# Kernel tuning notes

Measured on AMD Instinct MI355X. Metric: run time of the kernel, lower is better.

## Reference

```python
import jax, jax.numpy as jnp
import numpy as np

K = 3
PAD = 1
EPS = 1e-5


def _conv2d(x, w, b):
    y = jax.lax.conv_general_dilated(x, w, window_strides=(1, 1), padding='SAME',
                                     dimension_numbers=('NCHW', 'OIHW', 'NCHW'))
    return y + b[None, :, None, None]


def _bn(x, g, beta, m, v):
    inv = jax.lax.rsqrt(v + EPS)
    return (x - m[None, :, None, None]) * (g * inv)[None, :, None, None] + beta[None, :, None, None]


def _deform_conv2d(x, offset, w, b):
    # torchvision deform_conv2d (v1, no mask), stride=1, pad=1, 3x3 kernel.
    B, Cin, H, W = x.shape
    Cout = w.shape[0]
    # offset: [B, 2*K*K, H, W] -> (dy, dx) per kernel tap
    off = offset.reshape(B, K * K, 2, H, W)
    dy, dx = off[:, :, 0], off[:, :, 1]                     # [B, K2, H, W]
    ii, jj = jnp.meshgrid(jnp.arange(K), jnp.arange(K), indexing='ij')
    ki = (ii.reshape(-1) - PAD).astype(x.dtype)             # [K2]
    kj = (jj.reshape(-1) - PAD).astype(x.dtype)
    py = jnp.arange(H, dtype=x.dtype)[None, None, :, None] + ki[None, :, None, None] + dy
    px = jnp.arange(W, dtype=x.dtype)[None, None, None, :] + kj[None, :, None, None] + dx
    y0 = jnp.floor(py)
    x0 = jnp.floor(px)
    wy = py - y0
    wx = px - x0
    flat = x.reshape(B, Cin, H * W)

    def gather(yc, xc):
        valid = ((yc >= 0) & (yc < H) & (xc >= 0) & (xc < W)).astype(x.dtype)
        yi = jnp.clip(yc, 0, H - 1).astype(jnp.int32)
        xi = jnp.clip(xc, 0, W - 1).astype(jnp.int32)
        idx = (yi * W + xi).reshape(B, -1)                  # [B, K2*H*W]
        g = jax.vmap(lambda f, i: f[:, i])(flat, idx)       # [B, Cin, K2*H*W]
        return g.reshape(B, Cin, K * K, H, W) * valid[:, None]

    v = (gather(y0,     x0    ) * ((1 - wy) * (1 - wx))[:, None]
         + gather(y0,     x0 + 1) * ((1 - wy) * wx)[:, None]
         + gather(y0 + 1, x0    ) * (wy * (1 - wx))[:, None]
         + gather(y0 + 1, x0 + 1) * (wy * wx)[:, None])     # [B, Cin, K2, H, W]
    out = jnp.einsum('bckhw,ock->bohw', v, w.reshape(Cout, Cin, K * K))
    return out + b[None, :, None, None]


def setup_inputs() -> dict:
    key = jax.random.key(0)
    ks = jax.random.split(key, 12)
    d = {}
    d['x'] = jax.random.normal(ks[0], (32, 3, 64, 64), jnp.float32)
    d['offset1_w'] = jax.random.normal(ks[1], (18, 3, 3, 3), jnp.float32) * 0.05
    d['offset1_b'] = jnp.zeros((18,), jnp.float32)
    d['conv1_w'] = jax.random.normal(ks[2], (64, 3, 3, 3), jnp.float32) * 0.1
    d['conv1_b'] = jnp.zeros((64,), jnp.float32)
    d['bn1_gamma'] = jnp.ones((64,), jnp.float32)
    d['bn1_beta'] = jnp.zeros((64,), jnp.float32)
    d['bn1_mean'] = jnp.zeros((64,), jnp.float32)
    d['bn1_var'] = jax.random.uniform(ks[3], (64,), jnp.float32, 0.5, 1.5)
    d['offset2_w'] = jax.random.normal(ks[4], (18, 64, 3, 3), jnp.float32) * 0.02
    d['offset2_b'] = jnp.zeros((18,), jnp.float32)
    d['conv2_w'] = jax.random.normal(ks[5], (128, 64, 3, 3), jnp.float32) * 0.05
    d['conv2_b'] = jnp.zeros((128,), jnp.float32)
    d['bn2_gamma'] = jnp.ones((128,), jnp.float32)
    d['bn2_beta'] = jnp.zeros((128,), jnp.float32)
    d['bn2_mean'] = jnp.zeros((128,), jnp.float32)
    d['bn2_var'] = jax.random.uniform(ks[6], (128,), jnp.float32, 0.5, 1.5)
    d['fc1_w'] = jax.random.normal(ks[7], (256, 128), jnp.float32) * 0.08
    d['fc1_b'] = jnp.zeros((256,), jnp.float32)
    d['fc2_w'] = jax.random.normal(ks[8], (200, 256), jnp.float32) * 0.06
    d['fc2_b'] = jnp.zeros((200,), jnp.float32)
    return d


def reference(x, offset1_w, offset1_b, conv1_w, conv1_b, bn1_gamma, bn1_beta, bn1_mean, bn1_var,
              offset2_w, offset2_b, conv2_w, conv2_b, bn2_gamma, bn2_beta, bn2_mean, bn2_var,
              fc1_w, fc1_b, fc2_w, fc2_b):
    # Eval-mode forward (dropout layers are identity / deterministic).
    off1 = _conv2d(x, offset1_w, offset1_b)
    h = _deform_conv2d(x, off1, conv1_w, conv1_b)
    h = jax.nn.relu(_bn(h, bn1_gamma, bn1_beta, bn1_mean, bn1_var))
    off2 = _conv2d(h, offset2_w, offset2_b)
    h = _deform_conv2d(h, off2, conv2_w, conv2_b)
    h = jax.nn.relu(_bn(h, bn2_gamma, bn2_beta, bn2_mean, bn2_var))
    h = h.mean(axis=(2, 3))                                 # global avg pool -> [B, 128]
    h = jax.nn.relu(h @ fc1_w.T + fc1_b)
    return h @ fc2_w.T + fc2_b
```

## Files before the change

kernel.cpp:

```cpp
#include <hip/hip_runtime.h>

#define EPS 1e-5f

#define W1OT 0
#define W1B  1024
#define W2T  4096
#define W2OB 40960
#define SC1  59392
#define SH1  59456
#define SC2  59520
#define SH2  59648
#define POOL 59776
#define XP   65536
#define H1B  589824
#define W1B_U   2048
#define W2T_U   8192
#define W2OB_U  81920
#define H1B_U   1179648

typedef __attribute__((ext_vector_type(8))) short bhalf8;
typedef __attribute__((ext_vector_type(8))) unsigned short u16x8;
typedef __attribute__((ext_vector_type(4))) float f32x4;

#define APAD 40

struct Tap { int i00, i01, i10, i11; float w00, w01, w10, w11; };

__device__ __forceinline__ Tap make_tap(float py, float px) {
    float y0f = floorf(py), x0f = floorf(px);
    float wy = py - y0f, wx = px - x0f;
    bool by0 = (y0f >= 0.f)  && (y0f < 64.f);
    bool by1 = (y0f >= -1.f) && (y0f < 63.f);
    bool bx0 = (x0f >= 0.f)  && (x0f < 64.f);
    bool bx1 = (x0f >= -1.f) && (x0f < 63.f);
    int y0 = min(max((int)y0f, 0), 63);
    int y1 = min(max((int)y0f + 1, 0), 63);
    int x0 = min(max((int)x0f, 0), 63);
    int x1 = min(max((int)x0f + 1, 0), 63);
    Tap tp;
    tp.i00 = y0 * 64 + x0; tp.i01 = y0 * 64 + x1;
    tp.i10 = y1 * 64 + x0; tp.i11 = y1 * 64 + x1;
    tp.w00 = (by0 && bx0) ? (1.f - wy) * (1.f - wx) : 0.f;
    tp.w01 = (by0 && bx1) ? (1.f - wy) * wx         : 0.f;
    tp.w10 = (by1 && bx0) ? wy * (1.f - wx)         : 0.f;
    tp.w11 = (by1 && bx1) ? wy * wx                 : 0.f;
    return tp;
}

__device__ __forceinline__ ushort f2bf(float f) {
    union { float f; uint u; } a; a.f = f;
    uint u = a.u;
    return (ushort)((u + 0x7fffu + ((u >> 16) & 1u)) >> 16);
}
__device__ __forceinline__ float bf2f(ushort u) {
    union { uint u; float f; } a; a.u = ((uint)u) << 16;
    return a.f;
}

__device__ __forceinline__ f32x4 evenf(uint4 u) {
    union { uint u; float f; } a;
    f32x4 r;
    a.u = u.x << 16; r[0] = a.f;
    a.u = u.y << 16; r[1] = a.f;
    a.u = u.z << 16; r[2] = a.f;
    a.u = u.w << 16; r[3] = a.f;
    return r;
}
__device__ __forceinline__ f32x4 oddf(uint4 u) {
    union { uint u; float f; } a;
    f32x4 r;
    a.u = u.x & 0xffff0000u; r[0] = a.f;
    a.u = u.y & 0xffff0000u; r[1] = a.f;
    a.u = u.z & 0xffff0000u; r[2] = a.f;
    a.u = u.w & 0xffff0000u; r[3] = a.f;
    return r;
}

__device__ __forceinline__ void gl_lds16(const void* g, void* l) {
    __builtin_amdgcn_global_load_lds(
        (const __attribute__((address_space(1))) unsigned int*)g,
        (__attribute__((address_space(3))) unsigned int*)l, 16, 0, 0);
}

__global__ __launch_bounds__(256) void k_prep(
    const float* __restrict__ x,
    const float* __restrict__ o1w, const float* __restrict__ c1w,
    const float* __restrict__ o2w, const float* __restrict__ c2w,
    const float* __restrict__ c1b, const float* __restrict__ g1,
    const float* __restrict__ be1, const float* __restrict__ m1,
    const float* __restrict__ v1,
    const float* __restrict__ c2b, const float* __restrict__ g2,
    const float* __restrict__ be2, const float* __restrict__ m2,
    const float* __restrict__ v2,
    float* __restrict__ ws) {
    int tid = blockIdx.x * 256 + threadIdx.x;
    ushort* wsu = (ushort*)ws;
    if (tid < 648) {
        int co = tid % 18, tc = tid / 18, c = tc & 3, t = tc >> 2;
        ws[W1OT + tid] = (c < 3) ? o1w[(co * 3 + c) * 9 + t] : 0.f;
    } else if (tid < 2696) {
        int i = tid - 648;
        int n = i >> 5, k = i & 31;
        float v = 0.f;
        if (k < 27) { int c = k % 3, t = k / 3; v = c1w[(n * 3 + c) * 9 + t]; }
        wsu[W1B_U + i] = f2bf(v);
    } else if (tid < 76424) {
        int i = tid - 2696;
        int c = i & 63, n = (i >> 6) & 127, t = i >> 13;
        wsu[W2T_U + i] = f2bf(c2w[(n * 64 + c) * 9 + t]);
    } else if (tid < 94856) {
        int i = tid - 76424;
        int n = i / 576, k = i - n * 576;
        int c = k & 63, t = k >> 6;
        float v = (n < 18) ? o2w[(n * 64 + c) * 9 + t] : 0.f;
        wsu[W2OB_U + i] = f2bf(v);
    } else if (tid < 94920) {
        int i = tid - 94856;
        float s = g1[i] * rsqrtf(v1[i] + EPS);
        ws[SC1 + i] = s;
        ws[SH1 + i] = (c1b[i] - m1[i]) * s + be1[i];
    } else if (tid < 95048) {
        int i = tid - 94920;
        float s = g2[i] * rsqrtf(v2[i] + EPS);
        ws[SC2 + i] = s;
        ws[SH2 + i] = (c2b[i] - m2[i]) * s + be2[i];
    } else if (tid < 99144) {
        ws[POOL + tid - 95048] = 0.f;
    } else if (tid < 230216) {
        int i = tid - 99144;
        int b = i >> 12, hw = i & 4095;
        const float* xpp = x + (size_t)b * 3 * 4096 + hw;
        f32x4 o;
        o[0] = xpp[0]; o[1] = xpp[4096]; o[2] = xpp[8192]; o[3] = 0.f;
        *(f32x4*)(ws + XP + (size_t)i * 4) = o;
    }
}

__global__ __launch_bounds__(256, 4) void k_def1(
    const float* __restrict__ o1b, float* __restrict__ ws) {
    __shared__ ushort Alds[256 * APAD];
    __shared__ ushort Blds[64 * APAD];
    __shared__ float wo[648];
    __shared__ float scl[128];
    int tid = threadIdx.x;
    for (int i = tid; i < 648; i += 256) wo[i] = ws[W1OT + i];
    if (tid < 128) scl[tid] = ws[SC1 + tid];
    {
        const ushort* src = (const ushort*)ws + W1B_U;
        if (tid < 128) {
            int n = tid >> 1, half = (tid & 1) * 16;
            *(uint4*)(Blds + n * APAD + half)     = *(const uint4*)(src + n * 32 + half);
            *(uint4*)(Blds + n * APAD + half + 8) = *(const uint4*)(src + n * 32 + half + 8);
        }
    }
    int g = blockIdx.x;
    int b = (g & 7) * 4 + ((g >> 3) & 3);
    int row0 = (g >> 5) * 4;
    int h = row0 + (tid >> 6), w = tid & 63;
    const float* xp = ws + XP + (size_t)b * 16384;

    float off[18];
#pragma unroll
    for (int i = 0; i < 18; ++i) off[i] = o1b[i];
    __syncthreads();
#pragma unroll
    for (int t = 0; t < 9; ++t) {
        int yy = h + t / 3 - 1, xx = w + t % 3 - 1;
        f32x4 pv = (f32x4)0.f;
        if (yy >= 0 && yy < 64 && xx >= 0 && xx < 64)
            pv = *(const f32x4*)(xp + (yy * 64 + xx) * 4);
#pragma unroll
        for (int c = 0; c < 3; ++c) {
            const float* wp = wo + (t * 4 + c) * 18;
#pragma unroll
            for (int co = 0; co < 18; ++co) off[co] += pv[c] * wp[co];
        }
    }
    ushort ob[32];
#pragma unroll
    for (int i = 0; i < 32; ++i) ob[i] = 0;
#pragma unroll
    for (int t = 0; t < 9; ++t) {
        Tap tp = make_tap((float)(h + t / 3 - 1) + off[2 * t],
                          (float)(w + t % 3 - 1) + off[2 * t + 1]);
        f32x4 c00 = *(const f32x4*)(xp + tp.i00 * 4);
        f32x4 c01 = *(const f32x4*)(xp + tp.i01 * 4);
        f32x4 c10 = *(const f32x4*)(xp + tp.i10 * 4);
        f32x4 c11 = *(const f32x4*)(xp + tp.i11 * 4);
        f32x4 vt = tp.w00 * c00 + tp.w01 * c01 + tp.w10 * c10 + tp.w11 * c11;
        ob[t * 3 + 0] = f2bf(vt[0]);
        ob[t * 3 + 1] = f2bf(vt[1]);
        ob[t * 3 + 2] = f2bf(vt[2]);
    }
    {
        ushort* ar = Alds + tid * APAD;
#pragma unroll
        for (int i = 0; i < 4; ++i)
            *(uint4*)(ar + i * 8) = *(const uint4*)(ob + i * 8);
    }
    __syncthreads();

    int lane = tid & 63, wv = tid >> 6;
    int r = lane & 15, q = lane >> 4;
    bhalf8 bf[4];
#pragma unroll
    for (int nt = 0; nt < 4; ++nt)
        bf[nt] = *(const bhalf8*)(Blds + (nt * 16 + r) * APAD + q * 8);
    f32x4 acc[4][4];
#pragma unroll
    for (int mt = 0; mt < 4; ++mt) {
        bhalf8 af = *(const bhalf8*)(Alds + (wv * 64 + mt * 16 + r) * APAD + q * 8);
#pragma unroll
        for (int nt = 0; nt < 4; ++nt)
            acc[mt][nt] = __builtin_amdgcn_mfma_f32_16x16x32_bf16(af, bf[nt], (f32x4)0.f, 0, 0, 0);
    }
    ushort* hb = (ushort*)ws + H1B_U + (size_t)(b * 4096 + row0 * 64) * 64;
#pragma unroll
    for (int nt = 0; nt < 4; ++nt) {
        int col = nt * 16 + r;
        float s0 = scl[col], s1 = scl[64 + col];
#pragma unroll
        for (int mt = 0; mt < 4; ++mt) {
            int pxl = wv * 64 + mt * 16 + q * 4;
#pragma unroll
            for (int rr = 0; rr < 4; ++rr)
                hb[(size_t)(pxl + rr) * 64 + col] =
                    f2bf(fmaxf(acc[mt][nt][rr] * s0 + s1, 0.f));
        }
    }
}

__global__ __launch_bounds__(256, 4) void k_def2(
    const float* __restrict__ o2b, float* __restrict__ ws) {
    __shared__ ushort Bd[2][8192];
    __shared__ float offL[64 * 18];
    int g = blockIdx.x;
    int b = (g & 7) * 4 + ((g >> 3) & 3);
    int row = g >> 5;
    int tid = threadIdx.x, lane = tid & 63, wv = tid >> 6;
    int r = lane & 15, q = lane >> 4;
    int px = wv * 16 + r;
    const ushort* hb = (const ushort*)ws + H1B_U + (size_t)b * 262144;
    const ushort* wB = (const ushort*)ws + W2T_U;
    const ushort* bt = (const ushort*)ws + W2OB_U;

    {
        char* ldst = (char*)&Bd[0][0];
#pragma unroll
        for (int i = 0; i < 4; ++i) {
            int lin = wv * 4096 + i * 1024 + lane * 16;
            int src = lin ^ (((lin >> 7) & 7) << 4);
            gl_lds16((const char*)wB + src, ldst + wv * 4096 + i * 1024);
        }
    }

    f32x4 acc2[2];
    acc2[0] = (f32x4)0.f; acc2[1] = (f32x4)0.f;
#pragma unroll
    for (int t = 0; t < 9; ++t) {
        int yy = row + t / 3 - 1;
        int xx = px + t % 3 - 1;
        bool val = (yy >= 0 && yy < 64 && xx >= 0 && xx < 64);
        int yyc = min(max(yy, 0), 63), xxc = min(max(xx, 0), 63);
        const ushort* ap = hb + (size_t)(yyc * 64 + xxc) * 64 + q * 8;
#pragma unroll
        for (int ks = 0; ks < 2; ++ks) {
            bhalf8 af = val ? *(const bhalf8*)(ap + ks * 32) : (bhalf8)(short)0;
            int kk = t * 64 + ks * 32 + q * 8;
#pragma unroll
            for (int nt = 0; nt < 2; ++nt) {
                bhalf8 bf = *(const bhalf8*)(bt + (nt * 16 + r) * 576 + kk);
                acc2[nt] = __builtin_amdgcn_mfma_f32_16x16x32_bf16(af, bf, acc2[nt], 0, 0, 0);
            }
        }
    }
#pragma unroll
    for (int nt = 0; nt < 2; ++nt) {
        int n = nt * 16 + r;
        if (n < 18) {
            float bias = o2b[n];
#pragma unroll
            for (int rr = 0; rr < 4; ++rr)
                offL[(wv * 16 + q * 4 + rr) * 18 + n] = acc2[nt][rr] + bias;
        }
    }
    __syncthreads();

    f32x4 acc[8];
#pragma unroll
    for (int j = 0; j < 8; ++j) acc[j] = (f32x4)0.f;

    for (int t = 0; t < 9; ++t) {
        if (t < 8) {
            const char* wsrc = (const char*)wB + (t + 1) * 16384;
            char* ldst = (char*)&Bd[(t + 1) & 1][0];
#pragma unroll
            for (int i = 0; i < 4; ++i) {
                int lin = wv * 4096 + i * 1024 + lane * 16;
                int src = lin ^ (((lin >> 7) & 7) << 4);
                gl_lds16(wsrc + src, ldst + wv * 4096 + i * 1024);
            }
        }
        float oy = offL[px * 18 + 2 * t];
        float ox = offL[px * 18 + 2 * t + 1];
        Tap tp = make_tap((float)(row + t / 3 - 1) + oy,
                          (float)(px + t % 3 - 1) + ox);
        const ushort* Bq = Bd[t & 1];
#pragma unroll
        for (int ks = 0; ks < 2; ++ks) {
            int ko = ks * 32 + q * 8;
            uint4 u00 = *(const uint4*)(hb + (size_t)tp.i00 * 64 + ko);
            uint4 u01 = *(const uint4*)(hb + (size_t)tp.i01 * 64 + ko);
            uint4 u10 = *(const uint4*)(hb + (size_t)tp.i10 * 64 + ko);
            uint4 u11 = *(const uint4*)(hb + (size_t)tp.i11 * 64 + ko);
            f32x4 ve = tp.w00 * evenf(u00) + tp.w01 * evenf(u01)
                     + tp.w10 * evenf(u10) + tp.w11 * evenf(u11);
            f32x4 vo = tp.w00 * oddf(u00) + tp.w01 * oddf(u01)
                     + tp.w10 * oddf(u10) + tp.w11 * oddf(u11);
            union { uint u[4]; bhalf8 h; } A;
#pragma unroll
            for (int j = 0; j < 4; ++j)
                A.u[j] = (uint)f2bf(ve[j]) | ((uint)f2bf(vo[j]) << 16);
            bhalf8 bf[8];
#pragma unroll
            for (int nt = 0; nt < 8; ++nt) {
                int us = ((nt * 16 + r) * 64 + ko) ^ ((r & 7) << 3);
                bf[nt] = *(const bhalf8*)(Bq + us);
            }
#pragma unroll
            for (int nt = 0; nt < 8; ++nt)
                acc[nt] = __builtin_amdgcn_mfma_f32_16x16x32_bf16(A.h, bf[nt], acc[nt], 0, 0, 0);
        }
        if (t < 8) __syncthreads();
    }
    const float* sc = ws + SC2;
    const float* sh = ws + SH2;
    float* pool = ws + POOL;
#pragma unroll
    for (int nt = 0; nt < 8; ++nt) {
        int col = nt * 16 + r;
        float s0 = sc[col], s1 = sh[col];
        float s = 0.f;
#pragma unroll
        for (int rr = 0; rr < 4; ++rr)
            s += fmaxf(acc[nt][rr] * s0 + s1, 0.f);
        s += __shfl_xor(s, 16);
        s += __shfl_xor(s, 32);
        if (lane < 16) atomicAdd(&pool[b * 128 + col], s);
    }
}

__global__ __launch_bounds__(256) void k_fc(
    const float* __restrict__ w1, const float* __restrict__ b1,
    const float* __restrict__ w2, const float* __restrict__ b2,
    const float* __restrict__ ws, float* __restrict__ out) {
    int b = blockIdx.x, o = threadIdx.x;
    __shared__ float pl[128];
    __shared__ float hl[256];
    if (o < 128) pl[o] = ws[POOL + b * 128 + o] * (1.f / 4096.f);
    __syncthreads();
    float s = b1[o];
    const float* wp = w1 + o * 128;
#pragma unroll 8
    for (int c = 0; c < 128; ++c) s += pl[c] * wp[c];
    hl[o] = fmaxf(s, 0.f);
    __syncthreads();
    if (o < 200) {
        float s2 = b2[o];
        const float* wp2 = w2 + o * 256;
#pragma unroll 8
        for (int c = 0; c < 256; ++c) s2 += hl[c] * wp2[c];
        out[b * 200 + o] = s2;
    }
}

extern "C" void kernel_launch(void* const* d_in, const int* in_sizes, int n_in,
                              void* d_out, int out_size, void* d_ws, size_t ws_size,
                              hipStream_t stream) {
    const float* x   = (const float*)d_in[0];
    const float* o1w = (const float*)d_in[1];
    const float* o1b = (const float*)d_in[2];
    const float* c1w = (const float*)d_in[3];
    const float* c1b = (const float*)d_in[4];
    const float* g1  = (const float*)d_in[5];
    const float* be1 = (const float*)d_in[6];
    const float* m1  = (const float*)d_in[7];
    const float* v1  = (const float*)d_in[8];
    const float* o2w = (const float*)d_in[9];
    const float* o2b = (const float*)d_in[10];
    const float* c2w = (const float*)d_in[11];
    const float* c2b = (const float*)d_in[12];
    const float* g2  = (const float*)d_in[13];
    const float* be2 = (const float*)d_in[14];
    const float* m2  = (const float*)d_in[15];
    const float* v2  = (const float*)d_in[16];
    const float* f1w = (const float*)d_in[17];
    const float* f1b = (const float*)d_in[18];
    const float* f2w = (const float*)d_in[19];
    const float* f2b = (const float*)d_in[20];
    float* ws  = (float*)d_ws;
    float* out = (float*)d_out;

    k_prep<<<900, 256, 0, stream>>>(x, o1w, c1w, o2w, c2w,
                                    c1b, g1, be1, m1, v1,
                                    c2b, g2, be2, m2, v2, ws);
    k_def1<<<512, 256, 0, stream>>>(o1b, ws);
    k_def2<<<2048, 256, 0, stream>>>(o2b, ws);
    k_fc<<<32, 256, 0, stream>>>(f1w, f1b, f2w, f2b, ws, out);
}
```

Before: 308.5 us.

## Single-buffer def2 weight tiles, repack offset-conv weights, use hardware bf16 pack

The deformable conv2 kernel drops the double-buffered LDS weight tile for a single buffer and reuses it for the offsets, shrinking shared memory so occupancy can rise (launch bounds 4 to 6 blocks). All bilinear gather loads for a tap are issued before the weight tile load and blend, which hides gather latency behind the LDS fill, but adds a second barrier per tap and the weight prefetch no longer overlaps the previous tap's MFMAs. The offset-conv weights are pre-permuted so each lane reads a contiguous 16-byte chunk, and a single v_cvt_pk_bf16_f32 instruction replaces the software round-and-pack.

```diff
diff --git a/kernel.cpp b/kernel.cpp
--- a/kernel.cpp
+++ b/kernel.cpp
@@ -55,6 +55,12 @@
 __device__ __forceinline__ float bf2f(ushort u) {
     union { uint u; float f; } a; a.u = ((uint)u) << 16;
     return a.f;
+}
+
+__device__ __forceinline__ uint cvtpk_bf16(float a, float b) {
+    uint r;
+    asm("v_cvt_pk_bf16_f32 %0, %1, %2" : "=v"(r) : "v"(a), "v"(b));
+    return r;
 }
 
 __device__ __forceinline__ f32x4 evenf(uint4 u) {
@@ -110,8 +116,10 @@
         wsu[W2T_U + i] = f2bf(c2w[(n * 64 + c) * 9 + t]);
     } else if (tid < 94856) {
         int i = tid - 76424;
-        int n = i / 576, k = i - n * 576;
-        int c = k & 63, t = k >> 6;
+        int j = i & 7, r = (i >> 3) & 15, q = (i >> 7) & 3;
+        int nt = (i >> 9) & 1, ks = (i >> 10) & 1, t = i >> 11;
+        int n = nt * 16 + r;
+        int c = ks * 32 + q * 8 + j;
         float v = (n < 18) ? o2w[(n * 64 + c) * 9 + t] : 0.f;
         wsu[W2OB_U + i] = f2bf(v);
     } else if (tid < 94920) {
@@ -230,10 +238,11 @@
     }
 }
 
-__global__ __launch_bounds__(256, 4) void k_def2(
+__global__ __launch_bounds__(256, 6) void k_def2(
     const float* __restrict__ o2b, float* __restrict__ ws) {
-    __shared__ ushort Bd[2][8192];
-    __shared__ float offL[64 * 18];
+    __shared__ __align__(16) char smem[20992];
+    ushort* Bd  = (ushort*)smem;
+    float* offL = (float*)(smem + 16384);
     int g = blockIdx.x;
     int b = (g & 7) * 4 + ((g >> 3) & 3);
     int row = g >> 5;
@@ -242,17 +251,7 @@
     int px = wv * 16 + r;
     const ushort* hb = (const ushort*)ws + H1B_U + (size_t)b * 262144;
     const ushort* wB = (const ushort*)ws + W2T_U;
-    const ushort* bt = (const ushort*)ws + W2OB_U;
-
-    {
-        char* ldst = (char*)&Bd[0][0];
-#pragma unroll
-        for (int i = 0; i < 4; ++i) {
-            int lin = wv * 4096 + i * 1024 + lane * 16;
-            int src = lin ^ (((lin >> 7) & 7) << 4);
-            gl_lds16((const char*)wB + src, ldst + wv * 4096 + i * 1024);
-        }
-    }
+    const ushort* btl = (const ushort*)ws + W2OB_U + lane * 8;
 
     f32x4 acc2[2];
     acc2[0] = (f32x4)0.f; acc2[1] = (f32x4)0.f;
@@ -266,10 +265,9 @@
 #pragma unroll
         for (int ks = 0; ks < 2; ++ks) {
             bhalf8 af = val ? *(const bhalf8*)(ap + ks * 32) : (bhalf8)(short)0;
-            int kk = t * 64 + ks * 32 + q * 8;
 #pragma unroll
             for (int nt = 0; nt < 2; ++nt) {
-                bhalf8 bf = *(const bhalf8*)(bt + (nt * 16 + r) * 576 + kk);
+                bhalf8 bf = *(const bhalf8*)(btl + (size_t)((t * 2 + ks) * 2 + nt) * 512);
                 acc2[nt] = __builtin_amdgcn_mfma_f32_16x16x32_bf16(af, bf, acc2[nt], 0, 0, 0);
             }
         }
@@ -291,47 +289,57 @@
     for (int j = 0; j < 8; ++j) acc[j] = (f32x4)0.f;
 
     for (int t = 0; t < 9; ++t) {
-        if (t < 8) {
-            const char* wsrc = (const char*)wB + (t + 1) * 16384;
-            char* ldst = (char*)&Bd[(t + 1) & 1][0];
-#pragma unroll
-            for (int i = 0; i < 4; ++i) {
-                int lin = wv * 4096 + i * 1024 + lane * 16;
-                int src = lin ^ (((lin >> 7) & 7) << 4);
-                gl_lds16(wsrc + src, ldst + wv * 4096 + i * 1024);
-            }
-        }
+        if (t) __syncthreads();
         float oy = offL[px * 18 + 2 * t];
         float ox = offL[px * 18 + 2 * t + 1];
         Tap tp = make_tap((float)(row + t / 3 - 1) + oy,
                           (float)(px + t % 3 - 1) + ox);
-        const ushort* Bq = Bd[t & 1];
+        const ushort* p00 = hb + (size_t)tp.i00 * 64 + q * 8;
+        const ushort* p01 = hb + (size_t)tp.i01 * 64 + q * 8;
+        const ushort* p10 = hb + (size_t)tp.i10 * 64 + q * 8;
+        const ushort* p11 = hb + (size_t)tp.i11 * 64 + q * 8;
+        uint4 a00 = *(const uint4*)p00, b00 = *(const uint4*)(p00 + 32);
+        uint4 a01 = *(const uint4*)p01, b01 = *(const uint4*)(p01 + 32);
+        uint4 a10 = *(const uint4*)p10, b10 = *(const uint4*)(p10 + 32);
+        uint4 a11 = *(const uint4*)p11, b11 = *(const uint4*)(p11 + 32);
+        {
+            const char* wsrc = (const char*)wB + t * 16384;
+#pragma unroll
+            for (int i = 0; i < 4; ++i) {
+                int lin = wv * 4096 + i * 1024 + lane * 16;
+                int src = lin ^ (((lin >> 7) & 7) << 4);
+                gl_lds16(wsrc + src, smem + wv * 4096 + i * 1024);
+            }
+        }
+        union { uint u[4]; bhalf8 h; } A0, A1;
+        {
+            f32x4 ve = tp.w00 * evenf(a00) + tp.w01 * evenf(a01)
+                     + tp.w10 * evenf(a10) + tp.w11 * evenf(a11);
+            f32x4 vo = tp.w00 * oddf(a00) + tp.w01 * oddf(a01)
+                     + tp.w10 * oddf(a10) + tp.w11 * oddf(a11);
+#pragma unroll
+            for (int j = 0; j < 4; ++j) A0.u[j] = cvtpk_bf16(ve[j], vo[j]);
+        }
+        {
+            f32x4 ve = tp.w00 * evenf(b00) + tp.w01 * evenf(b01)
+                     + tp.w10 * evenf(b10) + tp.w11 * evenf(b11);
+            f32x4 vo = tp.w00 * oddf(b00) + tp.w01 * oddf(b01)
+                     + tp.w10 * oddf(b10) + tp.w11 * oddf(b11);
+#pragma unroll
+            for (int j = 0; j < 4; ++j) A1.u[j] = cvtpk_bf16(ve[j], vo[j]);
+        }
+        __syncthreads();
 #pragma unroll
         for (int ks = 0; ks < 2; ++ks) {
             int ko = ks * 32 + q * 8;
-            uint4 u00 = *(const uint4*)(hb + (size_t)tp.i00 * 64 + ko);
-            uint4 u01 = *(const uint4*)(hb + (size_t)tp.i01 * 64 + ko);
-            uint4 u10 = *(const uint4*)(hb + (size_t)tp.i10 * 64 + ko);
-            uint4 u11 = *(const uint4*)(hb + (size_t)tp.i11 * 64 + ko);
-            f32x4 ve = tp.w00 * evenf(u00) + tp.w01 * evenf(u01)
-                     + tp.w10 * evenf(u10) + tp.w11 * evenf(u11);
-            f32x4 vo = tp.w00 * oddf(u00) + tp.w01 * oddf(u01)
-                     + tp.w10 * oddf(u10) + tp.w11 * oddf(u11);
-            union { uint u[4]; bhalf8 h; } A;
-#pragma unroll
-            for (int j = 0; j < 4; ++j)
-                A.u[j] = (uint)f2bf(ve[j]) | ((uint)f2bf(vo[j]) << 16);
-            bhalf8 bf[8];
+            bhalf8 af = ks ? A1.h : A0.h;
 #pragma unroll
             for (int nt = 0; nt < 8; ++nt) {
                 int us = ((nt * 16 + r) * 64 + ko) ^ ((r & 7) << 3);
-                bf[nt] = *(const bhalf8*)(Bq + us);
+                bhalf8 bf = *(const bhalf8*)(Bd + us);
+                acc[nt] = __builtin_amdgcn_mfma_f32_16x16x32_bf16(af, bf, acc[nt], 0, 0, 0);
             }
-#pragma unroll
-            for (int nt = 0; nt < 8; ++nt)
-                acc[nt] = __builtin_amdgcn_mfma_f32_16x16x32_bf16(A.h, bf[nt], acc[nt], 0, 0, 0);
-        }
-        if (t < 8) __syncthreads();
+        }
     }
     const float* sc = ws + SC2;
     const float* sh = ws + SH2;
```

Result: slower. 388.7 us (+26.0%).
